# Optimization experiments

Hardware: AMD Instinct MI355X
Metric: run time of the kernel (lower is better)

The kernel has to match this reference:

```python
import jax, jax.numpy as jnp
import numpy as np

EMB = 8
HID = 64
B = 1000
T = 512
N = (B * T) // 5  # events per source; sources partition the (batch,time) grid

_KEYS = ["ccba", "cdtx", "cust", "dp", "remit"]
_NUMS = {"ccba": 8, "cdtx": 1, "cust": 1, "dp": 2, "remit": 1}
_CATS = {"ccba": 0, "cdtx": 2, "cust": 3, "dp": 8, "remit": 1}
_VOCAB = {"ccba": 0, "cdtx": 179, "cust": 37, "dp": 435, "remit": 5}


def setup_inputs() -> dict:
    ks = iter(jax.random.split(jax.random.key(0), 64))
    rng = np.random.default_rng(0)
    chunks = np.split(rng.permutation(B * T), 5)
    d = {}
    for k5, ch in zip(_KEYS, chunks):
        d[k5 + "_num"] = jax.random.normal(next(ks), (N, _NUMS[k5]), jnp.float32)
        if _CATS[k5] > 0:
            d[k5 + "_cat"] = jax.random.randint(next(ks), (N, _CATS[k5]), 0, _VOCAB[k5])
            d[k5 + "_tab"] = jax.random.normal(next(ks), (_VOCAB[k5], EMB), jnp.float32) * 0.1
        d[k5 + "_bi"] = jnp.asarray(ch // T, jnp.int32)
        d[k5 + "_ti"] = jnp.asarray(ch % T, jnp.int32)
        in_dim = _CATS[k5] * EMB + _NUMS[k5]
        d[k5 + "_W"] = jax.random.normal(next(ks), (in_dim, HID), jnp.float32) * np.float32(1.0 / np.sqrt(in_dim))
        d[k5 + "_b"] = jnp.zeros((HID,), jnp.float32)
    # LSTM: 2 layers x 2 directions, hidden 64, proj_size 1 -> layer1 input is 2
    for l, insz in [(0, HID), (1, 2)]:
        d[f"Wih{l}"] = jax.random.normal(next(ks), (2, 4 * HID, insz), jnp.float32) * 0.05
        d[f"Whh{l}"] = jax.random.normal(next(ks), (2, 4 * HID, 1), jnp.float32) * 0.05
        d[f"Whr{l}"] = jax.random.normal(next(ks), (2, 1, HID), jnp.float32) * 0.05
        d[f"bih{l}"] = jnp.zeros((2, 4 * HID), jnp.float32)
        d[f"bhh{l}"] = jnp.zeros((2, 4 * HID), jnp.float32)
    d["length"] = T
    d["batch_size"] = B
    return d


def _embed(num, cat, tab, W, b):
    # FeatureEmbedder: concat(categorical embeddings, numeric) -> Linear(hidden)
    x = num if cat is None else jnp.concatenate([tab[cat].reshape(cat.shape[0], -1), num], axis=-1)
    return x @ W + b


def _lstm_dir(x, Wih, Whh, Whr, bih, bhh, reverse):
    Bx = x.shape[0]
    H = Whr.shape[1]
    p = Whr.shape[0]
    bias = bih + bhh

    def step(carry, xt):
        h, c = carry  # h: [B,p] projected hidden, c: [B,H] cell
        g = xt @ Wih.T + h @ Whh.T + bias
        i, f, gg, o = jnp.split(g, 4, axis=-1)  # PyTorch gate order i,f,g,o
        c = jax.nn.sigmoid(f) * c + jax.nn.sigmoid(i) * jnp.tanh(gg)
        h = (jax.nn.sigmoid(o) * jnp.tanh(c)) @ Whr.T  # proj_size projection
        return (h, c), h

    init = (jnp.zeros((Bx, p), x.dtype), jnp.zeros((Bx, H), x.dtype))
    _, ys = jax.lax.scan(step, init, jnp.swapaxes(x, 0, 1), reverse=reverse)
    return jnp.swapaxes(ys, 0, 1)  # [B,T,p]


def _bilstm(x, Wih, Whh, Whr, bih, bhh):
    fwd = _lstm_dir(x, Wih[0], Whh[0], Whr[0], bih[0], bhh[0], False)
    bwd = _lstm_dir(x, Wih[1], Whh[1], Whr[1], bih[1], bhh[1], True)
    return jnp.concatenate([fwd, bwd], axis=-1)


def _forward(a):
    feat = jnp.zeros((a["batch_size"], a["length"], HID), jnp.float32)
    for k5 in _KEYS:
        v = _embed(a[k5 + "_num"], a.get(k5 + "_cat"), a.get(k5 + "_tab"), a[k5 + "_W"], a[k5 + "_b"])
        feat = feat.at[a[k5 + "_bi"], a[k5 + "_ti"]].set(v)  # scatter-assemble padded tensor
    h = _bilstm(feat, a["Wih0"], a["Whh0"], a["Whr0"], a["bih0"], a["bhh0"])
    h = _bilstm(h, a["Wih1"], a["Whh1"], a["Whr1"], a["bih1"], a["bhh1"])
    return h.mean(axis=2)  # [B,T]


def reference(ccba_num, ccba_bi, ccba_ti, ccba_W, ccba_b,
              cdtx_num, cdtx_cat, cdtx_tab, cdtx_bi, cdtx_ti, cdtx_W, cdtx_b,
              cust_num, cust_cat, cust_tab, cust_bi, cust_ti, cust_W, cust_b,
              dp_num, dp_cat, dp_tab, dp_bi, dp_ti, dp_W, dp_b,
              remit_num, remit_cat, remit_tab, remit_bi, remit_ti, remit_W, remit_b,
              Wih0, Whh0, Whr0, bih0, bhh0, Wih1, Whh1, Whr1, bih1, bhh1,
              length, batch_size):
    return _forward(dict(locals()))
```

## Files before the change

### kernel.cpp

```cpp
#include <hip/hip_runtime.h>
#include <cstdint>
#include <cstddef>

#define TLEN 512
#define BATCH 1000
#define NEV 102400
#define HID 64

__device__ __forceinline__ float fast_rcp(float x) {
#if __has_builtin(__builtin_amdgcn_rcpf)
    return __builtin_amdgcn_rcpf(x);
#else
    return 1.0f / x;
#endif
}
__device__ __forceinline__ float sigm(float x) { return fast_rcp(1.0f + __expf(-x)); }
__device__ __forceinline__ float tanh_f(float x) { return fmaf(2.0f, sigm(2.0f * x), -1.0f); }

__global__ __launch_bounds__(256) void embed_kernel(
    const float* __restrict__ num, const int* __restrict__ cat,
    const float* __restrict__ tab, const int* __restrict__ bi,
    const int* __restrict__ ti, const float* __restrict__ W,
    const float* __restrict__ bvec, float* __restrict__ feat,
    int n_num, int n_cat)
{
    int e = blockIdx.x * 4 + (threadIdx.x >> 6);
    int hh = threadIdx.x & 63;
    if (e >= NEV) return;
    float acc = bvec[hh];
    int j = 0;
    for (int c = 0; c < n_cat; ++c) {
        int idx = cat[e * n_cat + c];
        const float* trow = tab + (size_t)idx * 8;
#pragma unroll
        for (int u = 0; u < 8; ++u)
            acc = fmaf(trow[u], W[(j + u) * HID + hh], acc);
        j += 8;
    }
    for (int u = 0; u < n_num; ++u)
        acc = fmaf(num[(size_t)e * n_num + u], W[(j + u) * HID + hh], acc);
    int pos = bi[e] * TLEN + ti[e];
    feat[(size_t)pos * HID + hh] = acc;
}

__global__ __launch_bounds__(256) void lstm0_kernel(
    const float* __restrict__ feat, const float* __restrict__ Wih,
    const float* __restrict__ Whh, const float* __restrict__ Whr,
    const float* __restrict__ bih, const float* __restrict__ bhh,
    float* __restrict__ h0)
{
    int blk = blockIdx.x;
    int b = blk >> 1, dir = blk & 1;
    int tid = threadIdx.x, lane = tid & 63;

    const float* wrow = Wih + (size_t)(dir * 256 + tid) * HID;
    float4 w[16];
#pragma unroll
    for (int i = 0; i < 16; ++i) w[i] = ((const float4*)wrow)[i];
    float whh = Whh[dir * 256 + tid];
    float bias = bih[dir * 256 + tid] + bhh[dir * 256 + tid];
    float whr = Whr[dir * HID + lane];

    __shared__ float4 featb[2][16];
    __shared__ float gbuf[2][256];

    float c = 0.0f, h = 0.0f;
    const float* fb = feat + (size_t)b * TLEN * HID;

    int tt0 = dir ? (TLEN - 1) : 0;
    if (tid < 64) ((float*)featb[0])[tid] = fb[(size_t)tt0 * HID + tid];
    __syncthreads();

    for (int t = 0; t < TLEN; ++t) {
        int buf = t & 1;
        int tt = dir ? (TLEN - 1 - t) : t;
        float nf = 0.0f;
        int tn = dir ? (TLEN - 2 - t) : (t + 1);
        bool pf = (tid < 64) && (t < TLEN - 1);
        if (pf) nf = fb[(size_t)tn * HID + tid];

        float acc = fmaf(whh, h, bias);
#pragma unroll
        for (int i = 0; i < 16; ++i) {
            float4 f4 = featb[buf][i];
            acc = fmaf(f4.x, w[i].x, acc);
            acc = fmaf(f4.y, w[i].y, acc);
            acc = fmaf(f4.z, w[i].z, acc);
            acc = fmaf(f4.w, w[i].w, acc);
        }
        gbuf[buf][tid] = acc;
        if (pf) ((float*)featb[1 - buf])[tid] = nf;
        __syncthreads();

        float gi = gbuf[buf][lane];
        float gf = gbuf[buf][64 + lane];
        float gg = gbuf[buf][128 + lane];
        float go = gbuf[buf][192 + lane];
        c = sigm(gf) * c + sigm(gi) * tanh_f(gg);
        float p = sigm(go) * tanh_f(c) * whr;
#pragma unroll
        for (int off = 1; off < 64; off <<= 1) p += __shfl_xor(p, off, 64);
        h = p;
        if (tid == 0) h0[((size_t)b * TLEN + tt) * 2 + dir] = h;
    }
}

__global__ __launch_bounds__(256) void lstm1_kernel(
    const float* __restrict__ h0, const float* __restrict__ Wih,
    const float* __restrict__ Whh, const float* __restrict__ Whr,
    const float* __restrict__ bih, const float* __restrict__ bhh,
    float* __restrict__ h1)
{
    int w = threadIdx.x >> 6, lane = threadIdx.x & 63;
    int p = blockIdx.x * 4 + w;
    int b = p >> 1, dir = p & 1;

    float wi0[4], wi1[4], whh[4], bias[4];
#pragma unroll
    for (int k = 0; k < 4; ++k) {
        int r = k * 64 + lane;
        wi0[k] = Wih[(size_t)(dir * 256 + r) * 2 + 0];
        wi1[k] = Wih[(size_t)(dir * 256 + r) * 2 + 1];
        whh[k] = Whh[dir * 256 + r];
        bias[k] = bih[dir * 256 + r] + bhh[dir * 256 + r];
    }
    float whr = Whr[dir * HID + lane];
    float h = 0.0f, c = 0.0f;
    const float* hb = h0 + (size_t)b * TLEN * 2;

    for (int t = 0; t < TLEN; ++t) {
        int tt = dir ? (TLEN - 1 - t) : t;
        float x0 = hb[tt * 2], x1 = hb[tt * 2 + 1];
        float g[4];
#pragma unroll
        for (int k = 0; k < 4; ++k)
            g[k] = fmaf(whh[k], h, fmaf(wi1[k], x1, fmaf(wi0[k], x0, bias[k])));
        c = sigm(g[1]) * c + sigm(g[0]) * tanh_f(g[2]);
        float pp = sigm(g[3]) * tanh_f(c) * whr;
#pragma unroll
        for (int off = 1; off < 64; off <<= 1) pp += __shfl_xor(pp, off, 64);
        h = pp;
        if (lane == 0) h1[((size_t)b * TLEN + tt) * 2 + dir] = h;
    }
}

__global__ __launch_bounds__(256) void mean_kernel(
    const float2* __restrict__ h1, float* __restrict__ out)
{
    int i = blockIdx.x * 256 + threadIdx.x;
    if (i < BATCH * TLEN) {
        float2 v = h1[i];
        out[i] = 0.5f * (v.x + v.y);
    }
}

extern "C" void kernel_launch(void* const* d_in, const int* in_sizes, int n_in,
                              void* d_out, int out_size, void* d_ws, size_t ws_size,
                              hipStream_t stream)
{
    const float* ccba_num = (const float*)d_in[0];
    const int*   ccba_bi  = (const int*)d_in[1];
    const int*   ccba_ti  = (const int*)d_in[2];
    const float* ccba_W   = (const float*)d_in[3];
    const float* ccba_b   = (const float*)d_in[4];
    const float* cdtx_num = (const float*)d_in[5];
    const int*   cdtx_cat = (const int*)d_in[6];
    const float* cdtx_tab = (const float*)d_in[7];
    const int*   cdtx_bi  = (const int*)d_in[8];
    const int*   cdtx_ti  = (const int*)d_in[9];
    const float* cdtx_W   = (const float*)d_in[10];
    const float* cdtx_b   = (const float*)d_in[11];
    const float* cust_num = (const float*)d_in[12];
    const int*   cust_cat = (const int*)d_in[13];
    const float* cust_tab = (const float*)d_in[14];
    const int*   cust_bi  = (const int*)d_in[15];
    const int*   cust_ti  = (const int*)d_in[16];
    const float* cust_W   = (const float*)d_in[17];
    const float* cust_b   = (const float*)d_in[18];
    const float* dp_num   = (const float*)d_in[19];
    const int*   dp_cat   = (const int*)d_in[20];
    const float* dp_tab   = (const float*)d_in[21];
    const int*   dp_bi    = (const int*)d_in[22];
    const int*   dp_ti    = (const int*)d_in[23];
    const float* dp_W     = (const float*)d_in[24];
    const float* dp_b     = (const float*)d_in[25];
    const float* remit_num = (const float*)d_in[26];
    const int*   remit_cat = (const int*)d_in[27];
    const float* remit_tab = (const float*)d_in[28];
    const int*   remit_bi  = (const int*)d_in[29];
    const int*   remit_ti  = (const int*)d_in[30];
    const float* remit_W   = (const float*)d_in[31];
    const float* remit_b   = (const float*)d_in[32];
    const float* Wih0 = (const float*)d_in[33];
    const float* Whh0 = (const float*)d_in[34];
    const float* Whr0 = (const float*)d_in[35];
    const float* bih0 = (const float*)d_in[36];
    const float* bhh0 = (const float*)d_in[37];
    const float* Wih1 = (const float*)d_in[38];
    const float* Whh1 = (const float*)d_in[39];
    const float* Whr1 = (const float*)d_in[40];
    const float* bih1 = (const float*)d_in[41];
    const float* bhh1 = (const float*)d_in[42];

    char* ws = (char*)d_ws;
    float* feat = (float*)ws;
    float* h0   = (float*)(ws + 131072000);
    float* h1   = (float*)(ws + 135168000);
    float* out  = (float*)d_out;

    dim3 blk(256);
    int eg = (NEV + 3) / 4;

    embed_kernel<<<eg, blk, 0, stream>>>(ccba_num, nullptr, nullptr, ccba_bi, ccba_ti, ccba_W, ccba_b, feat, 8, 0);
    embed_kernel<<<eg, blk, 0, stream>>>(cdtx_num, cdtx_cat, cdtx_tab, cdtx_bi, cdtx_ti, cdtx_W, cdtx_b, feat, 1, 2);
    embed_kernel<<<eg, blk, 0, stream>>>(cust_num, cust_cat, cust_tab, cust_bi, cust_ti, cust_W, cust_b, feat, 1, 3);
    embed_kernel<<<eg, blk, 0, stream>>>(dp_num, dp_cat, dp_tab, dp_bi, dp_ti, dp_W, dp_b, feat, 2, 8);
    embed_kernel<<<eg, blk, 0, stream>>>(remit_num, remit_cat, remit_tab, remit_bi, remit_ti, remit_W, remit_b, feat, 1, 1);

    lstm0_kernel<<<BATCH * 2, blk, 0, stream>>>(feat, Wih0, Whh0, Whr0, bih0, bhh0, h0);
    lstm1_kernel<<<(BATCH * 2) / 4, blk, 0, stream>>>(h0, Wih1, Whh1, Whr1, bih1, bhh1, h1);
    mean_kernel<<<(BATCH * TLEN + 255) / 256, blk, 0, stream>>>((const float2*)h1, out);
}
```

Measured before the change: 1.625 ms.

## Process four batch rows per LSTM layer-0 block to reuse register weights

```diff
diff --git a/kernel.cpp b/kernel.cpp
--- a/kernel.cpp
+++ b/kernel.cpp
@@ -43,65 +43,87 @@
     feat[(size_t)pos * HID + hh] = acc;
 }
 
-__global__ __launch_bounds__(256) void lstm0_kernel(
+__global__ __launch_bounds__(256, 2) void lstm0_kernel(
     const float* __restrict__ feat, const float* __restrict__ Wih,
     const float* __restrict__ Whh, const float* __restrict__ Whr,
     const float* __restrict__ bih, const float* __restrict__ bhh,
     float* __restrict__ h0)
 {
-    int blk = blockIdx.x;
-    int b = blk >> 1, dir = blk & 1;
-    int tid = threadIdx.x, lane = tid & 63;
+    const int b0 = blockIdx.x * 4;
+    const int dir = blockIdx.y;
+    const int tid = threadIdx.x, lane = tid & 63, wv = tid >> 6;
 
     const float* wrow = Wih + (size_t)(dir * 256 + tid) * HID;
     float4 w[16];
 #pragma unroll
     for (int i = 0; i < 16; ++i) w[i] = ((const float4*)wrow)[i];
-    float whh = Whh[dir * 256 + tid];
-    float bias = bih[dir * 256 + tid] + bhh[dir * 256 + tid];
-    float whr = Whr[dir * HID + lane];
-
-    __shared__ float4 featb[2][16];
-    __shared__ float gbuf[2][256];
-
-    float c = 0.0f, h = 0.0f;
-    const float* fb = feat + (size_t)b * TLEN * HID;
-
-    int tt0 = dir ? (TLEN - 1) : 0;
-    if (tid < 64) ((float*)featb[0])[tid] = fb[(size_t)tt0 * HID + tid];
+    const float whh = Whh[dir * 256 + tid];
+    const float bias = bih[dir * 256 + tid] + bhh[dir * 256 + tid];
+    const float whr = Whr[dir * HID + lane];
+
+    __shared__ float4 featb[2][4][16];
+    __shared__ float gbuf[4][256];
+    __shared__ __align__(16) float hbuf[4];
+
+    float c = 0.0f;
+    const float* fb = feat + (size_t)(b0 + wv) * TLEN * HID;
+    float* h0b = h0 + ((size_t)(b0 + wv) * TLEN) * 2 + dir;
+
+    const int t0 = dir ? (TLEN - 1) : 0;
+    ((float*)featb[0][wv])[lane] = fb[(size_t)t0 * HID + lane];
+    if (tid < 4) hbuf[tid] = 0.0f;
     __syncthreads();
 
     for (int t = 0; t < TLEN; ++t) {
-        int buf = t & 1;
-        int tt = dir ? (TLEN - 1 - t) : t;
+        const int buf = t & 1;
+        const int tt = dir ? (TLEN - 1 - t) : t;
+
         float nf = 0.0f;
-        int tn = dir ? (TLEN - 2 - t) : (t + 1);
-        bool pf = (tid < 64) && (t < TLEN - 1);
-        if (pf) nf = fb[(size_t)tn * HID + tid];
-
-        float acc = fmaf(whh, h, bias);
+        const int tn = dir ? (TLEN - 2 - t) : (t + 1);
+        const bool pf = (t < TLEN - 1);
+        if (pf) nf = fb[(size_t)tn * HID + lane];
+
+        const float4 hp = *(const float4*)hbuf;
+
+        float a0 = fmaf(whh, hp.x, bias);
+        float a1 = fmaf(whh, hp.y, bias);
+        float a2 = fmaf(whh, hp.z, bias);
+        float a3 = fmaf(whh, hp.w, bias);
 #pragma unroll
         for (int i = 0; i < 16; ++i) {
-            float4 f4 = featb[buf][i];
-            acc = fmaf(f4.x, w[i].x, acc);
-            acc = fmaf(f4.y, w[i].y, acc);
-            acc = fmaf(f4.z, w[i].z, acc);
-            acc = fmaf(f4.w, w[i].w, acc);
+            float4 f0 = featb[buf][0][i];
+            float4 f1 = featb[buf][1][i];
+            float4 f2 = featb[buf][2][i];
+            float4 f3 = featb[buf][3][i];
+            a0 = fmaf(f0.x, w[i].x, a0); a0 = fmaf(f0.y, w[i].y, a0);
+            a0 = fmaf(f0.z, w[i].z, a0); a0 = fmaf(f0.w, w[i].w, a0);
+            a1 = fmaf(f1.x, w[i].x, a1); a1 = fmaf(f1.y, w[i].y, a1);
+            a1 = fmaf(f1.z, w[i].z, a1); a1 = fmaf(f1.w, w[i].w, a1);
+            a2 = fmaf(f2.x, w[i].x, a2); a2 = fmaf(f2.y, w[i].y, a2);
+            a2 = fmaf(f2.z, w[i].z, a2); a2 = fmaf(f2.w, w[i].w, a2);
+            a3 = fmaf(f3.x, w[i].x, a3); a3 = fmaf(f3.y, w[i].y, a3);
+            a3 = fmaf(f3.z, w[i].z, a3); a3 = fmaf(f3.w, w[i].w, a3);
         }
-        gbuf[buf][tid] = acc;
-        if (pf) ((float*)featb[1 - buf])[tid] = nf;
+        gbuf[0][tid] = a0;
+        gbuf[1][tid] = a1;
+        gbuf[2][tid] = a2;
+        gbuf[3][tid] = a3;
+        if (pf) ((float*)featb[1 - buf][wv])[lane] = nf;
         __syncthreads();
 
-        float gi = gbuf[buf][lane];
-        float gf = gbuf[buf][64 + lane];
-        float gg = gbuf[buf][128 + lane];
-        float go = gbuf[buf][192 + lane];
+        const float gi = gbuf[wv][lane];
+        const float gf = gbuf[wv][64 + lane];
+        const float gg = gbuf[wv][128 + lane];
+        const float go = gbuf[wv][192 + lane];
         c = sigm(gf) * c + sigm(gi) * tanh_f(gg);
         float p = sigm(go) * tanh_f(c) * whr;
 #pragma unroll
         for (int off = 1; off < 64; off <<= 1) p += __shfl_xor(p, off, 64);
-        h = p;
-        if (tid == 0) h0[((size_t)b * TLEN + tt) * 2 + dir] = h;
+        if (lane == 0) {
+            hbuf[wv] = p;
+            h0b[(size_t)tt * 2] = p;
+        }
+        __syncthreads();
     }
 }
 
@@ -217,7 +239,7 @@
     embed_kernel<<<eg, blk, 0, stream>>>(dp_num, dp_cat, dp_tab, dp_bi, dp_ti, dp_W, dp_b, feat, 2, 8);
     embed_kernel<<<eg, blk, 0, stream>>>(remit_num, remit_cat, remit_tab, remit_bi, remit_ti, remit_W, remit_b, feat, 1, 1);
 
-    lstm0_kernel<<<BATCH * 2, blk, 0, stream>>>(feat, Wih0, Whh0, Whr0, bih0, bhh0, h0);
+    lstm0_kernel<<<dim3(BATCH / 4, 2), blk, 0, stream>>>(feat, Wih0, Whh0, Whr0, bih0, bhh0, h0);
     lstm1_kernel<<<(BATCH * 2) / 4, blk, 0, stream>>>(h0, Wih1, Whh1, Whr1, bih1, bhh1, h1);
     mean_kernel<<<(BATCH * TLEN + 255) / 256, blk, 0, stream>>>((const float2*)h1, out);
 }
```

Result: faster. 1.567 ms (-3.6%).
